# Optimization experiments

Hardware: AMD Instinct MI355X
Metric: run time of the kernel (lower is better)

## Reference

```python
import jax, jax.numpy as jnp
import numpy as np
import math

D_MODEL = 1024
NUM_HEADS = 16
HEAD_DIM = D_MODEL // NUM_HEADS


def setup_inputs() -> dict:
    key = jax.random.key(0)
    ks = jax.random.split(key, 9)
    B, S = 2, 2048
    scale = 1.0 / math.sqrt(D_MODEL)
    x = jax.random.normal(ks[0], (B, S, D_MODEL), dtype=jnp.float32)
    # torch nn.Linear params: weight [out, in], bias [out]
    Wq = jax.random.normal(ks[1], (D_MODEL, D_MODEL), dtype=jnp.float32) * scale
    bq = jax.random.normal(ks[2], (D_MODEL,), dtype=jnp.float32) * scale
    Wk = jax.random.normal(ks[3], (D_MODEL, D_MODEL), dtype=jnp.float32) * scale
    bk = jax.random.normal(ks[4], (D_MODEL,), dtype=jnp.float32) * scale
    Wv = jax.random.normal(ks[5], (D_MODEL, D_MODEL), dtype=jnp.float32) * scale
    bv = jax.random.normal(ks[6], (D_MODEL,), dtype=jnp.float32) * scale
    Wo = jax.random.normal(ks[7], (D_MODEL, D_MODEL), dtype=jnp.float32) * scale
    bo = jax.random.normal(ks[8], (D_MODEL,), dtype=jnp.float32) * scale
    return {"x": x, "Wq": Wq, "bq": bq, "Wk": Wk, "bk": bk,
            "Wv": Wv, "bv": bv, "Wo": Wo, "bo": bo}


def reference(x, Wq, bq, Wk, bk, Wv, bv, Wo, bo):
    B, S, _ = x.shape
    H, Dh = NUM_HEADS, HEAD_DIM

    def proj(W, b):
        # torch Linear: x @ W.T + b -> [B,S,D] -> [B,H,S,Dh]
        y = jnp.einsum('bsd,ed->bse', x, W) + b
        return y.reshape(B, S, H, Dh).transpose(0, 2, 1, 3)

    Q = proj(Wq, bq)
    K = proj(Wk, bk)
    V = proj(Wv, bv)

    # scores [B,H,S,S], causal mask with -inf, then scale by 1/sqrt(head_dim)
    scores = jnp.einsum('bhqd,bhkd->bhqk', Q, K)
    causal = jnp.tril(jnp.ones((S, S), dtype=bool))
    scores = jnp.where(causal, scores, -jnp.inf)
    A = jax.nn.softmax(scores / math.sqrt(Dh), axis=-1)

    O = jnp.einsum('bhqk,bhkd->bhqd', A, V)  # [B,H,S,Dh]
    O = O.transpose(0, 2, 1, 3).reshape(B, S, H * Dh)
    return jnp.einsum('bsd,ed->bse', O, Wo) + bo
```

## Files before the change

kernel.cpp:

```cpp
#include <hip/hip_runtime.h>


typedef _Float16 f16x8 __attribute__((ext_vector_type(8)));
typedef _Float16 f16x4 __attribute__((ext_vector_type(4)));
typedef _Float16 f16x2 __attribute__((ext_vector_type(2)));
typedef float f32x4 __attribute__((ext_vector_type(4)));

#define S_  2048
#define DM  1024
#define NH  16
#define DH  64

__device__ __forceinline__ void gload_lds16(const void* g, void* s) {
  __builtin_amdgcn_global_load_lds(
      (const __attribute__((address_space(1))) void*)g,
      (__attribute__((address_space(3))) void*)s, 16, 0, 0);
}

__device__ __forceinline__ f16x2 pkrtz(float a, float b) {
  return __builtin_bit_cast(f16x2, __builtin_amdgcn_cvt_pkrtz(a, b));
}


__global__ void cvt_all_kernel(const float* __restrict__ x,
                               const float* __restrict__ w0,
                               const float* __restrict__ w1,
                               const float* __restrict__ w2,
                               const float* __restrict__ w3,
                               _Float16* __restrict__ xb,
                               _Float16* __restrict__ wb) {
  const int bid = blockIdx.x;
  const float* src;
  _Float16* dst;
  int idx;
  if (bid < 4096) {
    src = x; dst = xb; idx = bid * 256 + threadIdx.x;
  } else {
    const int j = bid - 4096;
    const int y = j >> 10;
    src = (y == 0) ? w0 : (y == 1) ? w1 : (y == 2) ? w2 : w3;
    dst = wb + (size_t)y * (DM * DM);
    idx = (j & 1023) * 256 + threadIdx.x;
  }
  const float4 v = ((const float4*)src)[idx];
  f16x4 h;
  h[0] = (_Float16)v.x; h[1] = (_Float16)v.y;
  h[2] = (_Float16)v.z; h[3] = (_Float16)v.w;
  ((f16x4*)dst)[idx] = h;
}


__global__ __launch_bounds__(256, 3) void gemm_qkv_kernel(
    const _Float16* __restrict__ xb, const _Float16* __restrict__ wb,
    const float* __restrict__ bq, const float* __restrict__ bk,
    const float* __restrict__ bv, _Float16* __restrict__ qkv)
{
  __shared__ _Float16 As[2][128 * 32];
  __shared__ _Float16 Ws[2][128 * 32];

  const int i = blockIdx.x;
  const int xcd = i & 7;
  const int tt = i >> 3;
  const int mp = xcd * 4 + (tt & 3);
  const int u = tt >> 2;
  const int np = u & 7;
  const int z = u >> 3;

  const _Float16* W = wb + (size_t)z * (DM * DM);
  const float* bias = (z == 0) ? bq : ((z == 1) ? bk : bv);
  _Float16* out = qkv + (size_t)z * 4194304;

  const f32x4 z4 = {0.f, 0.f, 0.f, 0.f};
  f32x4 acc[4][4];
#pragma unroll
  for (int mi = 0; mi < 4; ++mi)
#pragma unroll
    for (int ni = 0; ni < 4; ++ni) acc[mi][ni] = z4;

  const int m0 = mp * 128, n0 = np * 128;
  const int t = threadIdx.x;
  const int w = t >> 6, l = t & 63;
  const int quad = l >> 4, ln = l & 15;
  const int wm = (w >> 1) << 6, wn = (w & 1) << 6;
  const int srow = l >> 2, scol = (l & 3) << 3;

  for (int k0 = 0; k0 < DM; k0 += 64) {
#pragma unroll
    for (int h = 0; h < 2; ++h)
#pragma unroll
      for (int i2 = 0; i2 < 2; ++i2) {
        const int ra = w * 32 + i2 * 16;
        gload_lds16(&xb[(size_t)(m0 + ra + srow) * DM + k0 + h * 32 + scol],
                    &As[h][ra * 32]);
        gload_lds16(&W[(size_t)(n0 + ra + srow) * DM + k0 + h * 32 + scol],
                    &Ws[h][ra * 32]);
      }
    __syncthreads();

#pragma unroll
    for (int h = 0; h < 2; ++h) {
      f16x8 af[4], bf[4];
#pragma unroll
      for (int mi = 0; mi < 4; ++mi)
        af[mi] = *(const f16x8*)&As[h][(wm + mi * 16 + ln) * 32 + quad * 8];
#pragma unroll
      for (int ni = 0; ni < 4; ++ni)
        bf[ni] = *(const f16x8*)&Ws[h][(wn + ni * 16 + ln) * 32 + quad * 8];
#pragma unroll
      for (int mi = 0; mi < 4; ++mi)
#pragma unroll
        for (int ni = 0; ni < 4; ++ni)
          acc[mi][ni] = __builtin_amdgcn_mfma_f32_16x16x32_f16(
              af[mi], bf[ni], acc[mi][ni], 0, 0, 0);
    }
    __syncthreads();
  }

  const float scale = (z == 0) ? 0.18033688f : 1.0f;

#pragma unroll
  for (int ni = 0; ni < 4; ++ni) {
    const int c = n0 + wn + ni * 16 + ln;
    const float bias_c = bias[c];
    const int h = c >> 6, d = c & 63;
#pragma unroll
    for (int mi = 0; mi < 4; ++mi) {
      const int mb = m0 + wm + mi * 16 + quad * 4;
#pragma unroll
      for (int r = 0; r < 4; ++r) {
        const int mg = mb + r;
        const int b = mg >> 11, s = mg & 2047;
        const int bh = b * NH + h;
        const float v = (acc[mi][ni][r] + bias_c) * scale;
        size_t idx;
        if (z == 2)
          idx = (size_t)bh * 131072 + (s >> 5) * 2048 + (d >> 4) * 512 +
                ((s >> 3) & 3) * 128 + (d & 15) * 8 + (s & 7);
        else
          idx = (size_t)bh * 131072 + (s >> 4) * 1024 + (d >> 5) * 512 +
                ((d >> 3) & 3) * 128 + (s & 15) * 8 + (d & 7);
        out[idx] = (_Float16)v;
      }
    }
  }
}


__global__ __launch_bounds__(256, 2) void gemm_out_kernel(
    const _Float16* __restrict__ ob, const _Float16* __restrict__ wo,
    const float* __restrict__ bo, float* __restrict__ out)
{
  __shared__ _Float16 As[2][128 * 32];
  __shared__ _Float16 Ws[2][64 * 32];

  const int i = blockIdx.x;
  const int xcd = i & 7;
  const int tt = i >> 3;
  const int mp = xcd * 4 + (tt & 3);
  const int np = tt >> 2;

  const f32x4 z4 = {0.f, 0.f, 0.f, 0.f};
  f32x4 acc[2][4];
#pragma unroll
  for (int mi = 0; mi < 2; ++mi)
#pragma unroll
    for (int ni = 0; ni < 4; ++ni) acc[mi][ni] = z4;

  const int m0 = mp * 128, n0 = np * 64;
  const int t = threadIdx.x;
  const int w = t >> 6, l = t & 63;
  const int quad = l >> 4, ln = l & 15;
  const int srow = l >> 2, scol = (l & 3) << 3;

  for (int k0 = 0; k0 < DM; k0 += 64) {
#pragma unroll
    for (int h = 0; h < 2; ++h) {
#pragma unroll
      for (int i2 = 0; i2 < 2; ++i2) {
        const int ra = w * 32 + i2 * 16;
        gload_lds16(&ob[(size_t)(m0 + ra + srow) * DM + k0 + h * 32 + scol],
                    &As[h][ra * 32]);
      }
      gload_lds16(&wo[(size_t)(n0 + w * 16 + srow) * DM + k0 + h * 32 + scol],
                  &Ws[h][w * 16 * 32]);
    }
    __syncthreads();

#pragma unroll
    for (int h = 0; h < 2; ++h) {
      f16x8 af[2], bf[4];
#pragma unroll
      for (int mi = 0; mi < 2; ++mi)
        af[mi] = *(const f16x8*)&As[h][(w * 32 + mi * 16 + ln) * 32 + quad * 8];
#pragma unroll
      for (int ni = 0; ni < 4; ++ni)
        bf[ni] = *(const f16x8*)&Ws[h][(ni * 16 + ln) * 32 + quad * 8];
#pragma unroll
      for (int mi = 0; mi < 2; ++mi)
#pragma unroll
        for (int ni = 0; ni < 4; ++ni)
          acc[mi][ni] = __builtin_amdgcn_mfma_f32_16x16x32_f16(
              af[mi], bf[ni], acc[mi][ni], 0, 0, 0);
    }
    __syncthreads();
  }

#pragma unroll
  for (int ni = 0; ni < 4; ++ni) {
    const int c = n0 + ni * 16 + ln;
    const float bias_c = bo[c];
#pragma unroll
    for (int mi = 0; mi < 2; ++mi) {
      const int mb = m0 + w * 32 + mi * 16 + quad * 4;
#pragma unroll
      for (int r = 0; r < 4; ++r)
        out[(size_t)(mb + r) * DM + c] = acc[mi][ni][r] + bias_c;
    }
  }
}


__device__ __forceinline__ void ldkv(
    const _Float16* __restrict__ kb_, const _Float16* __restrict__ vb_,
    int t, int l, f16x8 (&kr)[4], f16x8 (&vr)[4])
{
#pragma unroll
  for (int ii = 0; ii < 4; ++ii)
    kr[ii] = *(const f16x8*)(kb_ + (size_t)t * 2048 + ii * 512 + l * 8);
#pragma unroll
  for (int ii = 0; ii < 4; ++ii)
    vr[ii] = *(const f16x8*)(vb_ + (size_t)t * 2048 + ii * 512 + l * 8);
}

template <int MODE>
__device__ __forceinline__ void compute64(
    const f16x8 (&kr)[4], const f16x8 (&vr)[4],
    const f16x8 (&qf)[4][2], f32x4 (&oacc)[4][4], float (&l_i)[4],
    _Float16* Ps, int quad, int ln)
{
  const f32x4 z4 = {0.f, 0.f, 0.f, 0.f};
#pragma unroll
  for (int qs = 0; qs < 4; ++qs) {
    if (MODE == 2 && qs < 2) continue;

    f32x4 sacc[2];
    sacc[0] = z4; sacc[1] = z4;
#pragma unroll
    for (int ks = 0; ks < 2; ++ks)
#pragma unroll
      for (int mi = 0; mi < 2; ++mi)
        sacc[mi] = __builtin_amdgcn_mfma_f32_16x16x32_f16(
            kr[mi * 2 + ks], qf[qs][ks], sacc[mi], 0, 0, 0);

    const bool DG = (MODE == 1 && qs < 2) || (MODE == 2);
    const int hq = ((MODE == 1) ? qs : (qs - 2)) << 4;

    float rs = 0.f;
#pragma unroll
    for (int mi = 0; mi < 2; ++mi) {
      float p[4];
#pragma unroll
      for (int r = 0; r < 4; ++r) {
        p[r] = __builtin_amdgcn_exp2f(sacc[mi][r]);
        if (DG && (mi * 16 + quad * 4 + r > hq + ln)) p[r] = 0.f;
        rs += p[r];
      }
      const f16x2 lo = pkrtz(p[0], p[1]);
      const f16x2 hi = pkrtz(p[2], p[3]);
      const f16x4 pk = __builtin_shufflevector(lo, hi, 0, 1, 2, 3);
      const int slot = ((mi * 4 + quad) + 2 * ln) & 15;
      *(f16x4*)&Ps[ln * 64 + slot * 4] = pk;
    }
    l_i[qs] += rs;

    const int slot2 = ((quad * 2) + 2 * ln) & 15;
    const f16x8 pb = *(const f16x8*)&Ps[ln * 64 + slot2 * 4];

#pragma unroll
    for (int di = 0; di < 4; ++di)
      oacc[qs][di] = __builtin_amdgcn_mfma_f32_16x16x32_f16(
          vr[di], pb, oacc[qs][di], 0, 0, 0);
  }
}

__global__ __launch_bounds__(256, 2) void attn_kernel(
    const _Float16* __restrict__ QF, const _Float16* __restrict__ KF,
    const _Float16* __restrict__ VF, _Float16* __restrict__ Ob)
{
  __shared__ _Float16 Ps[4][1024];
  __shared__ float mrgO[2][4][1024];
  __shared__ float mrgL[2][4][64];

  const int i = blockIdx.x;
  const int bh = i & 31;
  const int qb = 31 - (i >> 5);

  const int tid = threadIdx.x;
  const int e = tid >> 6, l = tid & 63;
  const int quad = l >> 4, ln = l & 15;

  const _Float16* qb_ = QF + (size_t)bh * 131072;
  const _Float16* kb_ = KF + (size_t)bh * 131072;
  const _Float16* vb_ = VF + (size_t)bh * 131072;
  _Float16* psw = &Ps[e][0];
  const int bidx = bh >> 4, hh = bh & 15;

  f16x8 qf[4][2];
#pragma unroll
  for (int qs = 0; qs < 4; ++qs)
#pragma unroll
    for (int ks = 0; ks < 2; ++ks)
      qf[qs][ks] = *(const f16x8*)
          (qb_ + (size_t)((4 * qb + qs) * 2 + ks) * 512 + l * 8);

  const f32x4 z4 = {0.f, 0.f, 0.f, 0.f};
  f32x4 oacc[4][4];
#pragma unroll
  for (int qs = 0; qs < 4; ++qs)
#pragma unroll
    for (int di = 0; di < 4; ++di) oacc[qs][di] = z4;
  float l_i[4] = {0.f, 0.f, 0.f, 0.f};

  f16x8 kr[4], vr[4];
  int t = e;
  if (t < 2 * qb) {
    ldkv(kb_, vb_, t, l, kr, vr);
    for (; t + 4 < 2 * qb; t += 4) {
      f16x8 kn[4], vn[4];
      ldkv(kb_, vb_, t + 4, l, kn, vn);
      compute64<0>(kr, vr, qf, oacc, l_i, psw, quad, ln);
#pragma unroll
      for (int ii = 0; ii < 4; ++ii) { kr[ii] = kn[ii]; vr[ii] = vn[ii]; }
    }
    compute64<0>(kr, vr, qf, oacc, l_i, psw, quad, ln);
  }
  if (((2 * qb) & 3) == e) {
    ldkv(kb_, vb_, 2 * qb, l, kr, vr);
    compute64<1>(kr, vr, qf, oacc, l_i, psw, quad, ln);
  }
  if (((2 * qb + 1) & 3) == e) {
    ldkv(kb_, vb_, 2 * qb + 1, l, kr, vr);
    compute64<2>(kr, vr, qf, oacc, l_i, psw, quad, ln);
  }

  if (e & 1) {
    const int buf = e >> 1;
#pragma unroll
    for (int qs = 0; qs < 4; ++qs) {
#pragma unroll
      for (int di = 0; di < 4; ++di)
        *(f32x4*)&mrgO[buf][qs][di * 256 + l * 4] = oacc[qs][di];
      mrgL[buf][qs][l] = l_i[qs];
    }
  }
  __syncthreads();
  if (!(e & 1)) {
    const int buf = e >> 1;
#pragma unroll
    for (int qs = 0; qs < 4; ++qs) {
#pragma unroll
      for (int di = 0; di < 4; ++di)
        oacc[qs][di] += *(const f32x4*)&mrgO[buf][qs][di * 256 + l * 4];
      l_i[qs] += mrgL[buf][qs][l];
    }
  }
  __syncthreads();
  if (e == 2) {
#pragma unroll
    for (int qs = 0; qs < 4; ++qs) {
#pragma unroll
      for (int di = 0; di < 4; ++di)
        *(f32x4*)&mrgO[0][qs][di * 256 + l * 4] = oacc[qs][di];
      mrgL[0][qs][l] = l_i[qs];
    }
  }
  __syncthreads();
  if (e == 0) {
#pragma unroll
    for (int qs = 0; qs < 4; ++qs) {
#pragma unroll
      for (int di = 0; di < 4; ++di)
        oacc[qs][di] += *(const f32x4*)&mrgO[0][qs][di * 256 + l * 4];
      float li = l_i[qs] + mrgL[0][qs][l];
      li += __shfl_xor(li, 16);
      li += __shfl_xor(li, 32);
      const float inv = 1.0f / li;

      const int q = qb * 64 + qs * 16 + ln;
      _Float16* orow = Ob + (size_t)(bidx * S_ + q) * DM + hh * DH + quad * 4;
#pragma unroll
      for (int di = 0; di < 4; ++di) {
        f16x4 o4;
#pragma unroll
        for (int r = 0; r < 4; ++r)
          o4[r] = (_Float16)(oacc[qs][di][r] * inv);
        *(f16x4*)(orow + di * 16) = o4;
      }
    }
  }
}


extern "C" void kernel_launch(void* const* d_in, const int* in_sizes, int n_in,
                              void* d_out, int out_size, void* d_ws, size_t ws_size,
                              hipStream_t stream) {
  (void)in_sizes; (void)n_in; (void)out_size; (void)ws_size;
  const float* x  = (const float*)d_in[0];
  const float* Wq = (const float*)d_in[1];
  const float* bq = (const float*)d_in[2];
  const float* Wk = (const float*)d_in[3];
  const float* bk = (const float*)d_in[4];
  const float* Wv = (const float*)d_in[5];
  const float* bv = (const float*)d_in[6];
  const float* Wo = (const float*)d_in[7];
  const float* bo = (const float*)d_in[8];

  char* ws = (char*)d_ws;
  _Float16* xb  = (_Float16*)(ws);
  _Float16* wb  = (_Float16*)(ws + (8u << 20));
  _Float16* qkv = (_Float16*)(ws + (16u << 20));
  _Float16* ob  = (_Float16*)(ws + (40u << 20));

  cvt_all_kernel<<<dim3(8192), dim3(256), 0, stream>>>(x, Wq, Wk, Wv, Wo, xb, wb);
  gemm_qkv_kernel<<<dim3(768), dim3(256), 0, stream>>>(xb, wb, bq, bk, bv, qkv);
  attn_kernel<<<dim3(1024), dim3(256), 0, stream>>>(
      qkv, qkv + 4194304, qkv + 2 * 4194304, ob);
  gemm_out_kernel<<<dim3(512), dim3(256), 0, stream>>>(
      ob, wb + (size_t)3 * DM * DM, bo, (float*)d_out);
}
```

Before: 168.5 us.

## Split attention KV loop across eight waves with deeper tree merge

Doubles the attention block to 512 threads so eight waves each handle every eighth 64-key tile instead of four waves handling every fourth. The per-wave P staging buffer is aliased onto the merge scratch space to save LDS, with an added barrier before the merge. The partial-output reduction becomes a three-level tree with more syncthreads. This shortens the per-block serial KV walk and adds wave-level parallelism, but it raises merge and synchronisation overhead and register pressure under launch_bounds(512,2).

New measurement: 181.7 us. 7.8% more time.

```diff
diff --git a/kernel.cpp b/kernel.cpp
--- a/kernel.cpp
+++ b/kernel.cpp
@@ -283,13 +283,13 @@
   }
 }
 
-__global__ __launch_bounds__(256, 2) void attn_kernel(
+__global__ __launch_bounds__(512, 2) void attn_kernel(
     const _Float16* __restrict__ QF, const _Float16* __restrict__ KF,
     const _Float16* __restrict__ VF, _Float16* __restrict__ Ob)
 {
-  __shared__ _Float16 Ps[4][1024];
   __shared__ float mrgO[2][4][1024];
   __shared__ float mrgL[2][4][64];
+  _Float16* Ps = (_Float16*)&mrgO[0][0][0];
 
   const int i = blockIdx.x;
   const int bh = i & 31;
@@ -302,7 +302,7 @@
   const _Float16* qb_ = QF + (size_t)bh * 131072;
   const _Float16* kb_ = KF + (size_t)bh * 131072;
   const _Float16* vb_ = VF + (size_t)bh * 131072;
-  _Float16* psw = &Ps[e][0];
+  _Float16* psw = Ps + e * 1024;
   const int bidx = bh >> 4, hh = bh & 15;
 
   f16x8 qf[4][2];
@@ -325,26 +325,28 @@
   int t = e;
   if (t < 2 * qb) {
     ldkv(kb_, vb_, t, l, kr, vr);
-    for (; t + 4 < 2 * qb; t += 4) {
+    for (; t + 8 < 2 * qb; t += 8) {
       f16x8 kn[4], vn[4];
-      ldkv(kb_, vb_, t + 4, l, kn, vn);
+      ldkv(kb_, vb_, t + 8, l, kn, vn);
       compute64<0>(kr, vr, qf, oacc, l_i, psw, quad, ln);
 #pragma unroll
       for (int ii = 0; ii < 4; ++ii) { kr[ii] = kn[ii]; vr[ii] = vn[ii]; }
     }
     compute64<0>(kr, vr, qf, oacc, l_i, psw, quad, ln);
   }
-  if (((2 * qb) & 3) == e) {
+  if (((2 * qb) & 7) == e) {
     ldkv(kb_, vb_, 2 * qb, l, kr, vr);
     compute64<1>(kr, vr, qf, oacc, l_i, psw, quad, ln);
   }
-  if (((2 * qb + 1) & 3) == e) {
+  if (((2 * qb + 1) & 7) == e) {
     ldkv(kb_, vb_, 2 * qb + 1, l, kr, vr);
     compute64<2>(kr, vr, qf, oacc, l_i, psw, quad, ln);
   }
 
-  if (e & 1) {
-    const int buf = e >> 1;
+  __syncthreads();
+
+  if (e == 1 || e == 5) {
+    const int buf = e >> 2;
 #pragma unroll
     for (int qs = 0; qs < 4; ++qs) {
 #pragma unroll
@@ -354,8 +356,8 @@
     }
   }
   __syncthreads();
-  if (!(e & 1)) {
-    const int buf = e >> 1;
+  if (e == 0 || e == 4) {
+    const int buf = e >> 2;
 #pragma unroll
     for (int qs = 0; qs < 4; ++qs) {
 #pragma unroll
@@ -365,7 +367,51 @@
     }
   }
   __syncthreads();
-  if (e == 2) {
+  if (e == 3 || e == 7) {
+    const int buf = e >> 2;
+#pragma unroll
+    for (int qs = 0; qs < 4; ++qs) {
+#pragma unroll
+      for (int di = 0; di < 4; ++di)
+        *(f32x4*)&mrgO[buf][qs][di * 256 + l * 4] = oacc[qs][di];
+      mrgL[buf][qs][l] = l_i[qs];
+    }
+  }
+  __syncthreads();
+  if (e == 2 || e == 6) {
+    const int buf = e >> 2;
+#pragma unroll
+    for (int qs = 0; qs < 4; ++qs) {
+#pragma unroll
+      for (int di = 0; di < 4; ++di)
+        oacc[qs][di] += *(const f32x4*)&mrgO[buf][qs][di * 256 + l * 4];
+      l_i[qs] += mrgL[buf][qs][l];
+    }
+  }
+  __syncthreads();
+  if (e == 2 || e == 6) {
+    const int buf = e >> 2;
+#pragma unroll
+    for (int qs = 0; qs < 4; ++qs) {
+#pragma unroll
+      for (int di = 0; di < 4; ++di)
+        *(f32x4*)&mrgO[buf][qs][di * 256 + l * 4] = oacc[qs][di];
+      mrgL[buf][qs][l] = l_i[qs];
+    }
+  }
+  __syncthreads();
+  if (e == 0 || e == 4) {
+    const int buf = e >> 2;
+#pragma unroll
+    for (int qs = 0; qs < 4; ++qs) {
+#pragma unroll
+      for (int di = 0; di < 4; ++di)
+        oacc[qs][di] += *(const f32x4*)&mrgO[buf][qs][di * 256 + l * 4];
+      l_i[qs] += mrgL[buf][qs][l];
+    }
+  }
+  __syncthreads();
+  if (e == 4) {
 #pragma unroll
     for (int qs = 0; qs < 4; ++qs) {
 #pragma unroll
@@ -423,7 +469,7 @@
 
   cvt_all_kernel<<<dim3(8192), dim3(256), 0, stream>>>(x, Wq, Wk, Wv, Wo, xb, wb);
   gemm_qkv_kernel<<<dim3(768), dim3(256), 0, stream>>>(xb, wb, bq, bk, bv, qkv);
-  attn_kernel<<<dim3(1024), dim3(256), 0, stream>>>(
+  attn_kernel<<<dim3(1024), dim3(512), 0, stream>>>(
       qkv, qkv + 4194304, qkv + 2 * 4194304, ob);
   gemm_out_kernel<<<dim3(512), dim3(256), 0, stream>>>(
       ob, wb + (size_t)3 * DM * DM, bo, (float*)d_out);
```
